# Kernel tuning notes

Measured on AMD Instinct MI355X. Metric: run time of the kernel, lower is better.

The kernel has to match this reference:

```python
import jax, jax.numpy as jnp
import numpy as np

NUM_BITS = 10
D_MODEL = 256
D_INNER = 512                      # expand=2 * hidden
D_STATE = 64
N_HEADS = 8                        # D_INNER // head_dim(64)
HEAD_DIM = 64
CONV_DIM = D_INNER + 2 * D_STATE   # 640
D_PROJ = D_INNER + CONV_DIM + N_HEADS  # 1160
KERNEL = 4
EPS = 1e-5
N_TOKENS = 16384


def _hilbert_code(coords):
    # coords: (N,3) int32 in [0, 2**NUM_BITS); Skilling's AxesToTranspose + bit interleave
    n = 3
    x = [coords[:, i] for i in range(n)]
    M = 1 << (NUM_BITS - 1)
    Q = M
    while Q > 1:
        P = Q - 1
        for i in range(n):
            cond = (x[i] & Q) > 0
            t = (x[0] ^ x[i]) & P
            x0_new = jnp.where(cond, x[0] ^ P, x[0] ^ t)
            xi_new = jnp.where(cond, x[i], x[i] ^ t)
            x[0] = x0_new
            if i > 0:
                x[i] = xi_new
        Q >>= 1
    for i in range(1, n):
        x[i] = x[i] ^ x[i - 1]
    t = jnp.zeros_like(x[0])
    Q = M
    while Q > 1:
        t = jnp.where((x[n - 1] & Q) > 0, t ^ (Q - 1), t)
        Q >>= 1
    x = [xi ^ t for xi in x]
    code = jnp.zeros_like(x[0])
    for b in range(NUM_BITS - 1, -1, -1):
        for i in range(n):
            code = (code << 1) | ((x[i] >> b) & 1)
    return code


def _serialized_orders(query_pos):
    # quantize to a 2**NUM_BITS grid, Hilbert-encode, sort ('hilbert' and 'hilbert-trans' = x/y swapped)
    pmin = query_pos.min(0)
    pmax = query_pos.max(0)
    g = ((query_pos - pmin) / (pmax - pmin + 1e-6) * (2 ** NUM_BITS - 1))
    g = jnp.clip(g, 0, 2 ** NUM_BITS - 1).astype(jnp.int32)
    orders, inverses = [], []
    for perm in ((0, 1, 2), (1, 0, 2)):
        code = _hilbert_code(g[:, jnp.array(perm)])
        o = jnp.argsort(code)
        orders.append(o)
        inverses.append(jnp.argsort(o))
    return orders, inverses


def _ln(x, w, b):
    m = x.mean(-1, keepdims=True)
    xc = x - m
    return xc * jax.lax.rsqrt(jnp.mean(xc * xc, -1, keepdims=True) + EPS) * w + b


def _mamba2(x, p):
    # x: (B, L, D_MODEL)
    B, L, _ = x.shape
    zxbcdt = x @ p['in_proj']                           # (B,L,1160)
    gate = zxbcdt[..., :D_INNER]
    xBC = zxbcdt[..., D_INNER:D_INNER + CONV_DIM]
    dt = zxbcdt[..., D_INNER + CONV_DIM:]               # (B,L,H)
    # causal depthwise conv over time
    xc = jnp.moveaxis(xBC, -1, 1)                       # (B,C,L)
    xc = jax.lax.conv_general_dilated(
        xc, p['conv_w'][:, None, :], window_strides=(1,),
        padding=[(KERNEL - 1, 0)], dimension_numbers=('NCH', 'OIH', 'NCH'),
        feature_group_count=CONV_DIM)
    xc = xc + p['conv_b'][None, :, None]
    xBC = jax.nn.silu(jnp.moveaxis(xc, 1, -1))          # (B,L,C)
    xs = xBC[..., :D_INNER].reshape(B, L, N_HEADS, HEAD_DIM)
    Bm = xBC[..., D_INNER:D_INNER + D_STATE]            # (B,L,S), n_groups=1 broadcast over heads
    Cm = xBC[..., D_INNER + D_STATE:]                   # (B,L,S)
    dt = jax.nn.softplus(dt + p['dt_bias'])             # (B,L,H)
    A = -jnp.exp(p['A_log'])                            # (H,)
    dA = jnp.exp(dt * A)                                # (B,L,H)

    def step(h, inp):
        dA_t, dt_t, x_t, B_t, C_t = inp                 # (B,H),(B,H),(B,H,P),(B,S),(B,S)
        h = h * dA_t[..., None, None] + (dt_t[..., None] * x_t)[..., None] * B_t[:, None, None, :]
        y = jnp.einsum('bhps,bs->bhp', h, C_t)
        return h, y

    tm = lambda a: jnp.moveaxis(a, 1, 0)
    h0 = jnp.zeros((B, N_HEADS, HEAD_DIM, D_STATE), x.dtype)
    _, ys = jax.lax.scan(step, h0, (tm(dA), tm(dt), tm(xs), tm(Bm), tm(Cm)))
    y = jnp.moveaxis(ys, 0, 1) + p['D'][None, None, :, None] * xs   # (B,L,H,P) + D skip
    y = y.reshape(B, L, D_INNER)
    # gated RMSNorm (MambaRMSNormGated)
    y = y * jax.nn.silu(gate)
    y = y * jax.lax.rsqrt(jnp.mean(y * y, -1, keepdims=True) + EPS) * p['norm_w']
    return y @ p['out_proj']                            # (B,L,D_MODEL)


def _forward(query, query_pos, pre_w, pre_b, fin_w, fin_b, layer_params):
    orders, invs = _serialized_orders(query_pos)
    q = query
    for p in layer_params:
        shortcut = q
        qn = _ln(q, pre_w, pre_b)
        stacked = jnp.stack([qn[orders[0]], qn[orders[1]]])   # (2, N, d) multi-path serialization
        y = _mamba2(stacked, p)
        q = shortcut + (y[0][invs[0]] + y[1][invs[1]]) * 0.5  # scatter back + average paths
        q = _ln(q, fin_w, fin_b)
    return q


def setup_inputs() -> dict:
    key = jax.random.key(0)
    ks = jax.random.split(key, 24)
    inp = {
        'query': jax.random.normal(ks[0], (N_TOKENS, D_MODEL), jnp.float32),
        'query_pos': jax.random.uniform(ks[1], (N_TOKENS, 3), jnp.float32),
        'pre_w': jnp.ones((D_MODEL,), jnp.float32),
        'pre_b': jnp.zeros((D_MODEL,), jnp.float32),
        'fin_w': jnp.ones((D_MODEL,), jnp.float32),
        'fin_b': jnp.zeros((D_MODEL,), jnp.float32),
    }
    for i in range(2):
        k = jax.random.split(ks[2 + i], 6)
        inp[f'in_proj{i}'] = jax.random.normal(k[0], (D_MODEL, D_PROJ), jnp.float32) * 0.02
        inp[f'conv_w{i}'] = jax.random.normal(k[1], (CONV_DIM, KERNEL), jnp.float32) * 0.2
        inp[f'conv_b{i}'] = jnp.zeros((CONV_DIM,), jnp.float32)
        inp[f'dt_bias{i}'] = jax.random.uniform(k[2], (N_HEADS,), jnp.float32, -4.0, -1.0)
        inp[f'A_log{i}'] = jnp.log(jnp.arange(1, N_HEADS + 1, dtype=jnp.float32))
        inp[f'D{i}'] = jnp.ones((N_HEADS,), jnp.float32)
        inp[f'norm_w{i}'] = jnp.ones((D_INNER,), jnp.float32)
        inp[f'out_proj{i}'] = jax.random.normal(k[3], (D_INNER, D_MODEL), jnp.float32) * 0.02
    return inp


def reference(query, query_pos, pre_w, pre_b, fin_w, fin_b,
              in_proj0, conv_w0, conv_b0, dt_bias0, A_log0, D0, norm_w0, out_proj0,
              in_proj1, conv_w1, conv_b1, dt_bias1, A_log1, D1, norm_w1, out_proj1):
    layer_params = [
        dict(in_proj=in_proj0, conv_w=conv_w0, conv_b=conv_b0, dt_bias=dt_bias0,
             A_log=A_log0, D=D0, norm_w=norm_w0, out_proj=out_proj0),
        dict(in_proj=in_proj1, conv_w=conv_w1, conv_b=conv_b1, dt_bias=dt_bias1,
             A_log=A_log1, D=D1, norm_w=norm_w1, out_proj=out_proj1),
    ]
    return _forward(query, query_pos, pre_w, pre_b, fin_w, fin_b, layer_params)
```

## Files before the change

kernel.cpp:

```cpp
#include <hip/hip_runtime.h>
#include <stdint.h>

#define L_TOK 16384
#define DM 256
#define DI 512
#define DS 64
#define NH 8
#define HD 64
#define CD 640
#define DP 1160
#define CHUNK 64
#define NC 256
#define EPSF 1e-5f

typedef __attribute__((ext_vector_type(8))) short short8;
typedef __attribute__((ext_vector_type(4))) float f32x4;

#define GLL16(gp, lp) __builtin_amdgcn_global_load_lds((const __attribute__((address_space(1))) void*)(gp), (__attribute__((address_space(3))) void*)(lp), 16, 0, 0)

__device__ __forceinline__ float warp_sum(float v) {
  v += __shfl_xor(v, 1, 64);
  v += __shfl_xor(v, 2, 64);
  v += __shfl_xor(v, 4, 64);
  v += __shfl_xor(v, 8, 64);
  v += __shfl_xor(v, 16, 64);
  v += __shfl_xor(v, 32, 64);
  return v;
}

__device__ __forceinline__ float siluf(float x) { return x / (1.0f + expf(-x)); }

__device__ __forceinline__ unsigned short f2bf(float f) {
  unsigned int u = __float_as_uint(f);
  unsigned int r = (u + 0x7FFFu + ((u >> 16) & 1u)) >> 16;
  return (unsigned short)r;
}
__device__ __forceinline__ float bf2f(unsigned short u) {
  return __uint_as_float(((unsigned int)u) << 16);
}


__global__ __launch_bounds__(256) void minmax_part(const float* __restrict__ pos, float* __restrict__ part) {
  __shared__ float sm[6][4];
  int tid = threadIdx.x;
  int t = blockIdx.x*256 + tid;
  float a = pos[t*3+0], b = pos[t*3+1], c = pos[t*3+2];
  float mn0=a, mn1=b, mn2=c, mx0=a, mx1=b, mx2=c;
  #pragma unroll
  for (int d = 1; d < 64; d <<= 1) {
    mn0=fminf(mn0,__shfl_xor(mn0,d,64));
    mn1=fminf(mn1,__shfl_xor(mn1,d,64));
    mn2=fminf(mn2,__shfl_xor(mn2,d,64));
    mx0=fmaxf(mx0,__shfl_xor(mx0,d,64));
    mx1=fmaxf(mx1,__shfl_xor(mx1,d,64));
    mx2=fmaxf(mx2,__shfl_xor(mx2,d,64));
  }
  if ((tid & 63) == 0) {
    int w = tid >> 6;
    sm[0][w]=mn0; sm[1][w]=mn1; sm[2][w]=mn2;
    sm[3][w]=mx0; sm[4][w]=mx1; sm[5][w]=mx2;
  }
  __syncthreads();
  if (tid < 6) {
    float r = sm[tid][0];
    if (tid < 3) { r=fminf(r,sm[tid][1]); r=fminf(r,sm[tid][2]); r=fminf(r,sm[tid][3]); }
    else         { r=fmaxf(r,sm[tid][1]); r=fmaxf(r,sm[tid][2]); r=fmaxf(r,sm[tid][3]); }
    part[blockIdx.x*6 + tid] = r;
  }
}

__global__ __launch_bounds__(64) void minmax_final(const float* __restrict__ part, float* __restrict__ pmm) {
  int tid = threadIdx.x;
  const float* p = part + tid*6;
  float mn0=p[0], mn1=p[1], mn2=p[2], mx0=p[3], mx1=p[4], mx2=p[5];
  #pragma unroll
  for (int d = 1; d < 64; d <<= 1) {
    mn0=fminf(mn0,__shfl_xor(mn0,d,64));
    mn1=fminf(mn1,__shfl_xor(mn1,d,64));
    mn2=fminf(mn2,__shfl_xor(mn2,d,64));
    mx0=fmaxf(mx0,__shfl_xor(mx0,d,64));
    mx1=fmaxf(mx1,__shfl_xor(mx1,d,64));
    mx2=fmaxf(mx2,__shfl_xor(mx2,d,64));
  }
  if (tid == 0) {
    pmm[0]=mn0; pmm[1]=mn1; pmm[2]=mn2;
    pmm[3]=mx0; pmm[4]=mx1; pmm[5]=mx2;
  }
}

__device__ unsigned int hilbert3(unsigned int a, unsigned int b, unsigned int c) {
  unsigned int x0 = a, x1 = b, x2 = c;
  for (unsigned int Q = 512u; Q > 1u; Q >>= 1) {
    unsigned int P = Q - 1u;
    { if (x0 & Q) x0 ^= P; }
    {
      unsigned int t = (x0 ^ x1) & P;
      if (x1 & Q) { x0 ^= P; }
      else { x0 ^= t; x1 ^= t; }
    }
    {
      unsigned int t = (x0 ^ x2) & P;
      if (x2 & Q) { x0 ^= P; }
      else { x0 ^= t; x2 ^= t; }
    }
  }
  x1 ^= x0; x2 ^= x1;
  unsigned int tt = 0;
  for (unsigned int Q = 512u; Q > 1u; Q >>= 1)
    if (x2 & Q) tt ^= (Q - 1u);
  x0 ^= tt; x1 ^= tt; x2 ^= tt;
  unsigned int code = 0;
  #pragma unroll
  for (int bb = 9; bb >= 0; --bb) {
    code = (code << 1) | ((x0 >> bb) & 1u);
    code = (code << 1) | ((x1 >> bb) & 1u);
    code = (code << 1) | ((x2 >> bb) & 1u);
  }
  return code;
}

__global__ __launch_bounds__(256) void hilbert_kernel(const float* __restrict__ pos, const float* __restrict__ pmm,
                                                      unsigned long long* __restrict__ keys) {
  int t = blockIdx.x*256 + threadIdx.x;
  if (t >= L_TOK) return;
  unsigned int g[3];
  #pragma unroll
  for (int d = 0; d < 3; ++d) {
    float v = (pos[t*3+d] - pmm[d]) / (pmm[3+d] - pmm[d] + 1e-6f) * 1023.0f;
    v = fminf(fmaxf(v, 0.0f), 1023.0f);
    g[d] = (unsigned int)(int)v;
  }
  unsigned int ca = hilbert3(g[0], g[1], g[2]);
  unsigned int cb = hilbert3(g[1], g[0], g[2]);
  keys[t]         = ((unsigned long long)ca << 14) | (unsigned long long)t;
  keys[L_TOK + t] = ((unsigned long long)cb << 14) | (unsigned long long)t;
}

__global__ __launch_bounds__(256) void rank_partial(const unsigned long long* __restrict__ keys,
                                                    unsigned int* __restrict__ partial) {
  __shared__ unsigned long long tile[512];
  int arr = blockIdx.y, ks = blockIdx.z;
  const unsigned long long* k = keys + (size_t)arr * L_TOK;
  int qbase = blockIdx.x*1024 + threadIdx.x;
  unsigned long long q[4];
  #pragma unroll
  for (int i = 0; i < 4; ++i) q[i] = k[qbase + 256*i];
  const unsigned long long* src = k + ks*512;
  #pragma unroll
  for (int t = 0; t < 2; ++t) tile[threadIdx.x + 256*t] = src[threadIdx.x + 256*t];
  __syncthreads();
  unsigned int r[4] = {};
  const ulonglong2* t2 = (const ulonglong2*)tile;
  #pragma unroll 4
  for (int j = 0; j < 256; ++j) {
    ulonglong2 v = t2[j];
    #pragma unroll
    for (int i = 0; i < 4; ++i) {
      r[i] += (v.x < q[i]) ? 1u : 0u;
      r[i] += (v.y < q[i]) ? 1u : 0u;
    }
  }
  #pragma unroll
  for (int i = 0; i < 4; ++i)
    partial[(size_t)(ks*2 + arr)*L_TOK + qbase + 256*i] = r[i];
}

__global__ __launch_bounds__(256) void rank_scatter(const unsigned long long* __restrict__ keys,
                                                    const unsigned int* __restrict__ partial,
                                                    unsigned int* __restrict__ ord,
                                                    unsigned int* __restrict__ inv) {
  int i = blockIdx.x*256 + threadIdx.x;
  int arr = i >> 14;
  int qi = i & (L_TOK - 1);
  unsigned int r = 0;
  #pragma unroll
  for (int ks = 0; ks < 32; ++ks) r += partial[(size_t)(ks*2 + arr)*L_TOK + qi];
  unsigned int tok = (unsigned int)(keys[i] & 0x3FFFu);
  ord[(size_t)arr*L_TOK + r] = tok;
  inv[(size_t)arr*L_TOK + tok] = r;
}


__global__ __launch_bounds__(256) void ln_kernel(const float* __restrict__ in, float* __restrict__ out,
                                                 unsigned short* __restrict__ outbf,
                                                 const float* __restrict__ w, const float* __restrict__ b) {
  int row = blockIdx.x*4 + (threadIdx.x >> 6);
  int lane = threadIdx.x & 63;
  const float4 v = *(const float4*)(in + (size_t)row*DM + lane*4);
  float s = v.x + v.y + v.z + v.w;
  float mean = warp_sum(s) * (1.0f/DM);
  float4 xc = make_float4(v.x-mean, v.y-mean, v.z-mean, v.w-mean);
  float ss = xc.x*xc.x + xc.y*xc.y + xc.z*xc.z + xc.w*xc.w;
  ss = warp_sum(ss) * (1.0f/DM);
  float inv = rsqrtf(ss + EPSF);
  const float4 w4 = *(const float4*)(w + lane*4);
  const float4 b4 = *(const float4*)(b + lane*4);
  float4 o;
  o.x = xc.x*inv*w4.x + b4.x;
  o.y = xc.y*inv*w4.y + b4.y;
  o.z = xc.z*inv*w4.z + b4.z;
  o.w = xc.w*inv*w4.w + b4.w;
  *(float4*)(out + (size_t)row*DM + lane*4) = o;
  if (outbf) {
    ushort4 ob = make_ushort4(f2bf(o.x), f2bf(o.y), f2bf(o.z), f2bf(o.w));
    *(ushort4*)(outbf + (size_t)row*DM + lane*4) = ob;
  }
}

__global__ __launch_bounds__(256) void lnfuse_kernel(float* __restrict__ io,
                                                     float* __restrict__ qn, unsigned short* __restrict__ qnbf,
                                                     const float* __restrict__ fw, const float* __restrict__ fb,
                                                     const float* __restrict__ pw, const float* __restrict__ pb) {
  int row = blockIdx.x*4 + (threadIdx.x >> 6);
  int lane = threadIdx.x & 63;
  const float4 v = *(const float4*)(io + (size_t)row*DM + lane*4);
  float s = v.x + v.y + v.z + v.w;
  float mean = warp_sum(s) * (1.0f/DM);
  float4 xc = make_float4(v.x-mean, v.y-mean, v.z-mean, v.w-mean);
  float ss = xc.x*xc.x + xc.y*xc.y + xc.z*xc.z + xc.w*xc.w;
  ss = warp_sum(ss) * (1.0f/DM);
  float inv = rsqrtf(ss + EPSF);
  const float4 w4 = *(const float4*)(fw + lane*4);
  const float4 b4 = *(const float4*)(fb + lane*4);
  float4 o;
  o.x = xc.x*inv*w4.x + b4.x;
  o.y = xc.y*inv*w4.y + b4.y;
  o.z = xc.z*inv*w4.z + b4.z;
  o.w = xc.w*inv*w4.w + b4.w;
  *(float4*)(io + (size_t)row*DM + lane*4) = o;
  if (qn) {
    float s2 = o.x + o.y + o.z + o.w;
    float mean2 = warp_sum(s2) * (1.0f/DM);
    float4 x2 = make_float4(o.x-mean2, o.y-mean2, o.z-mean2, o.w-mean2);
    float ss2 = x2.x*x2.x + x2.y*x2.y + x2.z*x2.z + x2.w*x2.w;
    ss2 = warp_sum(ss2) * (1.0f/DM);
    float inv2 = rsqrtf(ss2 + EPSF);
    const float4 pw4 = *(const float4*)(pw + lane*4);
    const float4 pb4 = *(const float4*)(pb + lane*4);
    float4 qv;
    qv.x = x2.x*inv2*pw4.x + pb4.x;
    qv.y = x2.y*inv2*pw4.y + pb4.y;
    qv.z = x2.z*inv2*pw4.z + pb4.z;
    qv.w = x2.w*inv2*pw4.w + pb4.w;
    *(float4*)(qn + (size_t)row*DM + lane*4) = qv;
    ushort4 qb = make_ushort4(f2bf(qv.x), f2bf(qv.y), f2bf(qv.z), f2bf(qv.w));
    *(ushort4*)(qnbf + (size_t)row*DM + lane*4) = qb;
  }
}


__global__ __launch_bounds__(256) void tcvt_both(const float* __restrict__ Wi, const float* __restrict__ Wo,
                                                 const float* __restrict__ nw,
                                                 unsigned short* __restrict__ WtA, unsigned short* __restrict__ WtO) {
  int idx = blockIdx.x*256 + threadIdx.x;
  if (idx < 1152*DM) {
    int n = idx >> 8, k = idx & 255;
    WtA[idx] = f2bf(Wi[(size_t)k*DP + n]);
  } else {
    int j = idx - 1152*DM;
    int n = j >> 9, k = j & 511;
    WtO[j] = f2bf(Wo[(size_t)k*DM + n] * nw[k]);
  }
}


__global__ __launch_bounds__(256) void gemm_in2(const unsigned short* __restrict__ Abf,
                                                const unsigned short* __restrict__ Wt,
                                                const unsigned int* __restrict__ ord,
                                                unsigned short* __restrict__ gate_nat,
                                                unsigned short* __restrict__ bcraw,
                                                unsigned short* __restrict__ xTg) {
  __shared__ unsigned short Alds[128*64];
  __shared__ unsigned short Blds[128*64];
  int tid = threadIdx.x, lane = tid & 63, w = tid >> 6;
  int bid = blockIdx.x;
  bool natp = bid < 640;
  int rb, cb, dir = 0, wcol0;
  if (natp) {
    int xcd = bid & 7, g = bid >> 3;
    rb = (xcd*16 + g/5)*128;
    cb = (g % 5)*128;
    wcol0 = cb;
  } else {
    int id = bid - 640;
    dir = id >> 9;
    int b = id & 511;
    int xcd = b & 7, g = b >> 3;
    rb = (xcd*16 + g/4)*128;
    cb = (g % 4)*128;
    wcol0 = DI + cb;
  }
  int wm = (w & 1)*64, wn = (w >> 1)*64;
  const unsigned int* ordp = ord + (size_t)dir*L_TOK;
  const unsigned short* pA[4]; const unsigned short* pB[4];
  unsigned short* dA[4]; unsigned short* dB[4];
  #pragma unroll
  for (int s = 0; s < 4; ++s) {
    int inst = w*4 + s;
    int r = inst*8 + (lane >> 3);
    int cA = (lane & 7) ^ (r & 7);
    int arow = natp ? (rb + r) : (int)ordp[rb + r];
    pA[s] = Abf + (size_t)arow*DM + cA*8;
    pB[s] = Wt + (size_t)(wcol0 + r)*DM + cA*8;
    dA[s] = &Alds[inst*512];
    dB[s] = &Blds[inst*512];
  }
  f32x4 zero = {0.f, 0.f, 0.f, 0.f};
  f32x4 acc[4][4];
  #pragma unroll
  for (int i = 0; i < 4; ++i)
    #pragma unroll
    for (int j = 0; j < 4; ++j) acc[i][j] = zero;
  int t = lane & 15, q = lane >> 4;
  for (int k0 = 0; k0 < DM; k0 += 64) {
    #pragma unroll
    for (int s = 0; s < 4; ++s) GLL16(pA[s] + k0, dA[s]);
    #pragma unroll
    for (int s = 0; s < 4; ++s) GLL16(pB[s] + k0, dB[s]);
    __syncthreads();
    #pragma unroll
    for (int ks = 0; ks < 2; ++ks) {
      short8 af[4], bfr[4];
      int cc = ks*4 + q;
      #pragma unroll
      for (int i = 0; i < 4; ++i) {
        int rr = wm + 16*i + t;
        af[i] = *(const short8*)&Alds[rr*64 + ((cc ^ (rr & 7))*8)];
      }
      #pragma unroll
      for (int j = 0; j < 4; ++j) {
        int rr = wn + 16*j + t;
        bfr[j] = *(const short8*)&Blds[rr*64 + ((cc ^ (rr & 7))*8)];
      }
      #pragma unroll
      for (int i = 0; i < 4; ++i)
        #pragma unroll
        for (int j = 0; j < 4; ++j)
          acc[i][j] = __builtin_amdgcn_mfma_f32_16x16x32_bf16(af[i], bfr[j], acc[i][j], 0, 0, 0);
    }
    __syncthreads();
  }
  if (natp) {
    unsigned short* dst; int ld;
    if (cb < DI) { dst = gate_nat + cb; ld = DI; }
    else         { dst = bcraw + (cb - DI); ld = 128; }
    #pragma unroll
    for (int i = 0; i < 4; ++i) {
      int rowb = rb + wm + 16*i + q*4;
      #pragma unroll
      for (int j = 0; j < 4; ++j) {
        int col = wn + 16*j + t;
        #pragma unroll
        for (int r = 0; r < 4; ++r)
          dst[(size_t)(rowb + r)*ld + col] = f2bf(acc[i][j][r]);
      }
    }
  } else {
    #pragma unroll
    for (int i = 0; i < 4; ++i) {
      int rowb = rb + wm + 16*i + q*4;
      #pragma unroll
      for (int j = 0; j < 4; ++j) {
        int col = wn + 16*j + t;
        ushort4 o = make_ushort4(f2bf(acc[i][j][0]), f2bf(acc[i][j][1]),
                                 f2bf(acc[i][j][2]), f2bf(acc[i][j][3]));
        *(ushort4*)(xTg + (size_t)(cb + col)*(2*L_TOK) + (size_t)dir*L_TOK + rowb) = o;
      }
    }
  }
}


__global__ __launch_bounds__(256) void gemm_out_gather(const unsigned short* __restrict__ ybuf,
                                                       const unsigned short* __restrict__ Wt,
                                                       const unsigned int* __restrict__ inv,
                                                       const float* __restrict__ rms_acc,
                                                       const float* __restrict__ shortcut,
                                                       float* __restrict__ out) {
  __shared__ unsigned short Alds[2*64*64];
  __shared__ unsigned short Blds[128*64];
  int tid = threadIdx.x, lane = tid & 63, w = tid >> 6;
  int bid = blockIdx.x;
  int xcd = bid & 7, g = bid >> 3;
  int rb = (xcd*32 + (g >> 1))*64;
  int cb = (g & 1)*128;
  int wm = (w & 1)*32, wn = (w >> 1)*64;
  const unsigned short* pA0[2]; const unsigned short* pA1[2];
  unsigned short* dA0[2]; unsigned short* dA1[2];
  const unsigned short* pB[4]; unsigned short* dB[4];
  #pragma unroll
  for (int s = 0; s < 2; ++s) {
    int inst = w*2 + s;
    int r = inst*8 + (lane >> 3);
    int cA = (lane & 7) ^ (r & 7);
    int tok = rb + r;
    pA0[s] = ybuf + (size_t)inv[tok]*DI + cA*8;
    pA1[s] = ybuf + (size_t)L_TOK*DI + (size_t)inv[L_TOK + tok]*DI + cA*8;
    dA0[s] = &Alds[inst*512];
    dA1[s] = &Alds[4096 + inst*512];
  }
  #pragma unroll
  for (int s = 0; s < 4; ++s) {
    int inst = w*4 + s;
    int r = inst*8 + (lane >> 3);
    int cA = (lane & 7) ^ (r & 7);
    pB[s] = Wt + (size_t)(cb + r)*DI + cA*8;
    dB[s] = &Blds[inst*512];
  }
  f32x4 zero = {0.f, 0.f, 0.f, 0.f};
  f32x4 acc0[2][4], acc1[2][4];
  #pragma unroll
  for (int i = 0; i < 2; ++i)
    #pragma unroll
    for (int j = 0; j < 4; ++j) { acc0[i][j] = zero; acc1[i][j] = zero; }
  int t = lane & 15, q = lane >> 4;
  for (int k0 = 0; k0 < DI; k0 += 64) {
    #pragma unroll
    for (int s = 0; s < 2; ++s) { GLL16(pA0[s] + k0, dA0[s]); GLL16(pA1[s] + k0, dA1[s]); }
    #pragma unroll
    for (int s = 0; s < 4; ++s) GLL16(pB[s] + k0, dB[s]);
    __syncthreads();
    #pragma unroll
    for (int ks = 0; ks < 2; ++ks) {
      short8 af0[2], af1[2], bfr[4];
      int cc = ks*4 + q;
      #pragma unroll
      for (int i = 0; i < 2; ++i) {
        int rr = wm + 16*i + t;
        int off = rr*64 + ((cc ^ (rr & 7))*8);
        af0[i] = *(const short8*)&Alds[off];
        af1[i] = *(const short8*)&Alds[4096 + off];
      }
      #pragma unroll
      for (int j = 0; j < 4; ++j) {
        int rr = wn + 16*j + t;
        bfr[j] = *(const short8*)&Blds[rr*64 + ((cc ^ (rr & 7))*8)];
      }
      #pragma unroll
      for (int i = 0; i < 2; ++i)
        #pragma unroll
        for (int j = 0; j < 4; ++j) {
          acc0[i][j] = __builtin_amdgcn_mfma_f32_16x16x32_bf16(af0[i], bfr[j], acc0[i][j], 0, 0, 0);
          acc1[i][j] = __builtin_amdgcn_mfma_f32_16x16x32_bf16(af1[i], bfr[j], acc1[i][j], 0, 0, 0);
        }
    }
    __syncthreads();
  }
  #pragma unroll
  for (int i = 0; i < 2; ++i) {
    #pragma unroll
    for (int r = 0; r < 4; ++r) {
      int row = rb + wm + 16*i + q*4 + r;
      float ir0 = rsqrtf(rms_acc[row]*(1.0f/DI) + EPSF);
      float ir1 = rsqrtf(rms_acc[L_TOK + row]*(1.0f/DI) + EPSF);
      const float* sp = shortcut + (size_t)row*DM + cb;
      float* op = out + (size_t)row*DM + cb;
      #pragma unroll
      for (int j = 0; j < 4; ++j) {
        int col = wn + 16*j + t;
        op[col] = sp[col] + 0.5f*(ir0*acc0[i][j][r] + ir1*acc1[i][j][r]);
      }
    }
  }
}


__global__ __launch_bounds__(256) void dtconv(const float* __restrict__ qn, const float* __restrict__ W,
                                              const float* __restrict__ dt_bias, float* __restrict__ dtb,
                                              float* __restrict__ rms_acc,
                                              const unsigned short* __restrict__ bcraw,
                                              const float* __restrict__ cw, const float* __restrict__ cbias,
                                              const unsigned int* __restrict__ ord,
                                              unsigned short* __restrict__ bcswz,
                                              unsigned short* __restrict__ bcswzA) {
  __shared__ unsigned short smem[131*64];
  int tid = threadIdx.x;
  int bx = blockIdx.x;
  if (bx < 512) {
    int gid = bx*256 + tid;
    if (gid < 2*L_TOK) rms_acc[gid] = 0.f;
    float* Wl = (float*)smem;
    {
      const float* wp = W + (size_t)tid*DP + (DI + CD);
      float4 wa = *(const float4*)wp;
      float4 wb = *(const float4*)(wp + 4);
      int off = tid*8 + (tid >> 5)*4;
      *(float4*)&Wl[off]     = wa;
      *(float4*)&Wl[off + 4] = wb;
    }
    __syncthreads();
    int lane = tid & 63, w = tid >> 6;
    int r = bx*32 + w*8 + (lane >> 3);
    int kg = lane & 7;
    const float* qp = qn + (size_t)r*DM + kg*32;
    float acc[8] = {};
    #pragma unroll
    for (int i = 0; i < 8; ++i) {
      float4 q4 = *(const float4*)(qp + i*4);
      float qv[4] = {q4.x, q4.y, q4.z, q4.w};
      #pragma unroll
      for (int e = 0; e < 4; ++e) {
        int k = kg*32 + i*4 + e;
        int off = k*8 + kg*4;
        float4 wa = *(const float4*)&Wl[off];
        float4 wb = *(const float4*)&Wl[off + 4];
        acc[0] = fmaf(qv[e], wa.x, acc[0]);
        acc[1] = fmaf(qv[e], wa.y, acc[1]);
        acc[2] = fmaf(qv[e], wa.z, acc[2]);
        acc[3] = fmaf(qv[e], wa.w, acc[3]);
        acc[4] = fmaf(qv[e], wb.x, acc[4]);
        acc[5] = fmaf(qv[e], wb.y, acc[5]);
        acc[6] = fmaf(qv[e], wb.z, acc[6]);
        acc[7] = fmaf(qv[e], wb.w, acc[7]);
      }
    }
    #pragma unroll
    for (int h = 0; h < 8; ++h) {
      acc[h] += __shfl_xor(acc[h], 8, 64);
      acc[h] += __shfl_xor(acc[h], 16, 64);
      acc[h] += __shfl_xor(acc[h], 32, 64);
    }
    float v = 0.f;
    #pragma unroll
    for (int h = 0; h < 8; ++h) if (kg == h) v = acc[h];
    v += dt_bias[kg];
    float sp = (v > 0.0f) ? (v + log1pf(expf(-v))) : log1pf(expf(v));
    dtb[(size_t)r*NH + kg] = sp;
  } else {
    int cid = bx - 512;
    int half = cid & 1, ty = (cid >> 1) & 127, dir = cid >> 8;
    unsigned short* tile = smem;
    const unsigned int* ordp = ord + (size_t)dir*L_TOK;
    int ch0 = DI + half*64;
    int co0 = half*64;
    int t0 = ty*128;
    for (int cc = tid; cc < 131*8; cc += 256) {
      int r = cc >> 3, cgc = cc & 7;
      int t = t0 - 3 + r;
      short8 v = {0,0,0,0,0,0,0,0};
      if (t >= 0) v = *(const short8*)(bcraw + (size_t)ordp[t]*128 + co0 + cgc*8);
      *(short8*)&tile[r*64 + ((cgc ^ (r & 7))*8)] = v;
    }
    int cg = tid & 7, tp = tid >> 3;
    int ch = ch0 + cg*8;
    float wv[8][4];
    float bias[8];
    #pragma unroll
    for (int e = 0; e < 8; ++e) {
      float4 c4 = *(const float4*)(cw + (ch + e)*4);
      wv[e][0] = c4.x; wv[e][1] = c4.y; wv[e][2] = c4.z; wv[e][3] = c4.w;
    }
    {
      float4 b0 = *(const float4*)(cbias + ch);
      float4 b1 = *(const float4*)(cbias + ch + 4);
      bias[0]=b0.x; bias[1]=b0.y; bias[2]=b0.z; bias[3]=b0.w;
      bias[4]=b1.x; bias[5]=b1.y; bias[6]=b1.z; bias[7]=b1.w;
    }
    __syncthreads();
    #pragma unroll
    for (int tk = 0; tk < 4; ++tk) {
      int rel = tp + 32*tk;
      float acc[8];
      #pragma unroll
      for (int e = 0; e < 8; ++e) acc[e] = bias[e];
      #pragma unroll
      for (int k = 0; k < 4; ++k) {
        int r = rel + k;
        short8 v = *(const short8*)&tile[r*64 + ((cg ^ (r & 7))*8)];
        #pragma unroll
        for (int e = 0; e < 8; ++e)
          acc[e] = fmaf(wv[e][k], bf2f((unsigned short)v[e]), acc[e]);
      }
      short8 o;
      #pragma unroll
      for (int e = 0; e < 8; ++e) o[e] = (short)f2bf(siluf(acc[e]));
      int T = t0 + rel;
      int chn = T >> 6, tl = T & 63;
      unsigned short* tb = bcswz + ((size_t)((dir*NC + chn)*2 + half))*4096;
      *(short8*)(tb + tl*64 + ((cg ^ (tl & 7))*8)) = o;
      if (half == 0) {
        unsigned short* ta = bcswzA + ((size_t)(dir*NC + chn))*4096;
        #pragma unroll
        for (int e = 0; e < 8; ++e) {
          int s5 = cg*8 + e;
          ta[s5*64 + (((tl >> 3) ^ (s5 & 7))*8) + (tl & 7)] = (unsigned short)o[e];
        }
      }
    }
  }
}


__global__ __launch_bounds__(256) void phaseA_mfma(const unsigned short* __restrict__ xTg,
                                                   const unsigned short* __restrict__ bcswzA,
                                                   const float* __restrict__ cw, const float* __restrict__ cbias,
                                                   const float* __restrict__ dtb, const float* __restrict__ A_log,
                                                   const unsigned int* __restrict__ ord,
                                                   unsigned short* __restrict__ S, float* __restrict__ P,
                                                   unsigned short* __restrict__ xsT) {
  int c = blockIdx.x, h = blockIdx.y, dir = blockIdx.z, tid = threadIdx.x;
  int lane = tid & 63, w = tid >> 6;
  int hh = dir*NH + h;
  __shared__ unsigned short xT[64*64];
  __shared__ unsigned short Bt[64*64];
  __shared__ float wgt[64];
  int c0 = c*CHUNK;
  float Ah = -expf(A_log[h]);
  const unsigned short* bA = bcswzA + ((size_t)(dir*NC + c))*4096;
  #pragma unroll
  for (int s = 0; s < 2; ++s) {
    int inst = w*2 + s;
    GLL16(bA + (size_t)inst*512 + lane*8, &Bt[inst*512]);
  }
  if (tid < 64) {
    unsigned int tok = ord[(size_t)dir*L_TOK + c0 + tid];
    float dtv = dtb[(size_t)tok*NH + h];
    float v = dtv*Ah;
    float s = v;
    #pragma unroll
    for (int d = 1; d < 64; d <<= 1) {
      float u = __shfl_down(s, d, 64);
      s += (tid + d < 64) ? u : 0.f;
    }
    wgt[tid] = dtv*expf(s - v);
    if (tid == 0) P[hh*NC + c] = expf(s);
  }
  __syncthreads();
  unsigned short* xpg = xsT + ((size_t)(hh*NC + c))*4096;
  #pragma unroll
  for (int i = 0; i < 2; ++i) {
    int q = tid + 256*i;
    int p = q >> 3, tg = q & 7;
    int sw8 = (tg ^ (p & 7))*8;
    const unsigned short* xrow = xTg + (size_t)(h*HD + p)*(2*L_TOK) + (size_t)dir*L_TOK;
    int tb = c0 + tg*8;
    short8 cur = *(const short8*)(xrow + tb);
    short8 prv = {0,0,0,0,0,0,0,0};
    if (tb >= 8) prv = *(const short8*)(xrow + tb - 8);
    float4 w4 = *(const float4*)(cw + (size_t)(h*HD + p)*4);
    float bb = cbias[h*HD + p];
    float xv[11];
    xv[0] = bf2f((unsigned short)prv[5]);
    xv[1] = bf2f((unsigned short)prv[6]);
    xv[2] = bf2f((unsigned short)prv[7]);
    #pragma unroll
    for (int k = 0; k < 8; ++k) xv[3+k] = bf2f((unsigned short)cur[k]);
    short8 raw, wtd;
    #pragma unroll
    for (int k = 0; k < 8; ++k) {
      float a = bb + w4.x*xv[k] + w4.y*xv[k+1] + w4.z*xv[k+2] + w4.w*xv[k+3];
      unsigned short rbf = f2bf(siluf(a));
      raw[k] = (short)rbf;
      wtd[k] = (short)f2bf(bf2f(rbf)*wgt[tg*8 + k]);
    }
    *(short8*)(xpg + p*64 + sw8) = raw;
    *(short8*)&xT[p*64 + sw8] = wtd;
  }
  __syncthreads();
  int t16 = lane & 15, q4 = lane >> 4;
  f32x4 zero = {0.f,0.f,0.f,0.f};
  f32x4 acc[4];
  #pragma unroll
  for (int j = 0; j < 4; ++j) acc[j] = zero;
  #pragma unroll
  for (int ks = 0; ks < 2; ++ks) {
    int rowA = 16*w + t16;
    short8 a = *(const short8*)&xT[rowA*64 + (((ks*4 + q4) ^ (rowA & 7))*8)];
    #pragma unroll
    for (int j = 0; j < 4; ++j) {
      int rowB = 16*j + t16;
      short8 b = *(const short8*)&Bt[rowB*64 + (((ks*4 + q4) ^ (rowB & 7))*8)];
      acc[j] = __builtin_amdgcn_mfma_f32_16x16x32_bf16(a, b, acc[j], 0, 0, 0);
    }
  }
  unsigned short* Sp = S + ((size_t)(hh*NC + c))*4096;
  #pragma unroll
  for (int j = 0; j < 4; ++j)
    #pragma unroll
    for (int r = 0; r < 4; ++r) {
      int row = 16*w + q4*4 + r;
      int cg2 = 2*j + (t16 >> 3);
      Sp[(size_t)row*64 + (((cg2 ^ (row & 7)) << 3) | (t16 & 7))] = f2bf(acc[j][r]);
    }
}


__global__ __launch_bounds__(128) void phaseB_scan(unsigned short* __restrict__ S, const float* __restrict__ P) {
  __shared__ float Pl[NC];
  int b = blockIdx.x;
  int hh = b >> 4;
  int e2 = (b & 15)*128 + threadIdx.x;
  for (int i = threadIdx.x; i < NC; i += 128) Pl[i] = P[hh*NC + i];
  __syncthreads();
  unsigned int* base = (unsigned int*)(S + ((size_t)hh*NC)*4096) + e2;
  float hx = 0.f, hy = 0.f;
  #pragma unroll 1
  for (int k0 = 0; k0 < NC; k0 += 16) {
    unsigned int v[16];
    #pragma unroll
    for (int u = 0; u < 16; ++u) v[u] = base[(size_t)(k0+u)*2048];
    #pragma unroll
    for (int u = 0; u < 16; ++u) {
      float p = Pl[k0+u];
      unsigned int old = v[u];
      base[(size_t)(k0+u)*2048] = (unsigned int)f2bf(hx) | ((unsigned int)f2bf(hy) << 16);
      hx = p*hx + bf2f((unsigned short)(old & 0xffffu));
      hy = p*hy + bf2f((unsigned short)(old >> 16));
    }
  }
}

__global__ __launch_bounds__(256) void phaseC_mfma(const unsigned short* __restrict__ bcswz,
                                                   const unsigned short* __restrict__ xsT,
                                                   const unsigned short* __restrict__ gate_nat,
                                                   const float* __restrict__ dtb, const float* __restrict__ A_log,
                                                   const float* __restrict__ Dp,
                                                   const unsigned int* __restrict__ ord,
                                                   const unsigned short* __restrict__ S,
                                                   unsigned short* __restrict__ ybuf,
                                                   float* __restrict__ rms_acc) {
  int c = blockIdx.x, h = blockIdx.y, dir = blockIdx.z, tid = threadIdx.x;
  int lane = tid & 63, w = tid >> 6;
  int hh = dir*NH + h;
  unsigned short* y = ybuf + (size_t)dir*L_TOK*DI;
  __shared__ unsigned short Cl[64*64];
  __shared__ unsigned short Bl[64*64];
  __shared__ unsigned short h0l[64*64];
  __shared__ unsigned short xT[64*64];
  __shared__ float dts[64], pl[64], pe[64];
  int c0 = c*CHUNK;
  float Ah = -expf(A_log[h]);
  float Dh = Dp[h];
  const unsigned short* Sp = S + ((size_t)(hh*NC + c))*4096;
  const unsigned short* xp = xsT + ((size_t)(hh*NC + c))*4096;
  const unsigned short* Bg = bcswz + ((size_t)((dir*NC + c)*2 + 0))*4096;
  const unsigned short* Cg = bcswz + ((size_t)((dir*NC + c)*2 + 1))*4096;
  #pragma unroll
  for (int s = 0; s < 2; ++s) {
    int inst = w*2 + s;
    GLL16(Sp + (size_t)inst*512 + lane*8, &h0l[inst*512]);
    GLL16(xp + (size_t)inst*512 + lane*8, &xT[inst*512]);
    GLL16(Bg + (size_t)inst*512 + lane*8, &Bl[inst*512]);
    GLL16(Cg + (size_t)inst*512 + lane*8, &Cl[inst*512]);
  }
  if (tid < 64) {
    unsigned int tok = ord[(size_t)dir*L_TOK + c0 + tid];
    float dtv = dtb[(size_t)tok*NH + h];
    dts[tid] = dtv;
    float v = dtv*Ah;
    float s = v;
    #pragma unroll
    for (int d = 1; d < 64; d <<= 1) {
      float u = __shfl_up(s, d, 64);
      s += (tid >= d) ? u : 0.f;
    }
    pl[tid] = s;
    pe[tid] = expf(s);
  }
  __syncthreads();
  int t16 = lane & 15, q4 = lane >> 4;
  int t0 = 16*w;
  f32x4 zero = {0.f,0.f,0.f,0.f};
  f32x4 accG[4], accY[4];
  #pragma unroll
  for (int j = 0; j < 4; ++j) { accG[j] = zero; accY[j] = zero; }
  #pragma unroll
  for (int ks = 0; ks < 2; ++ks) {
    int rowA = t0 + t16;
    short8 a = *(const short8*)&Cl[rowA*64 + (((ks*4 + q4) ^ (rowA & 7))*8)];
    #pragma unroll
    for (int j = 0; j < 4; ++j) {
      int rowB = 16*j + t16;
      int off = rowB*64 + (((ks*4 + q4) ^ (rowB & 7))*8);
      accG[j] = __builtin_amdgcn_mfma_f32_16x16x32_bf16(a, *(const short8*)&Bl[off], accG[j], 0, 0, 0);
      accY[j] = __builtin_amdgcn_mfma_f32_16x16x32_bf16(a, *(const short8*)&h0l[off], accY[j], 0, 0, 0);
    }
  }
  #pragma unroll
  for (int j = 0; j < 4; ++j) {
    #pragma unroll
    for (int r = 0; r < 4; ++r) {
      int t = t0 + q4*4 + r;
      int s = 16*j + t16;
      float v = 0.f;
      if (s <= t) {
        v = accG[j][r] * dts[s] * expf(pl[t] - pl[s]);
        if (s == t) v += Dh;
      }
      Cl[t*64 + (((s >> 3) ^ (t & 7))*8 + (s & 7))] = f2bf(v);
    }
  }
  unsigned int tokr[4];
  #pragma unroll
  for (int r = 0; r < 4; ++r) tokr[r] = ord[(size_t)dir*L_TOK + c0 + t0 + q4*4 + r];
  float gv[4][4];
  #pragma unroll
  for (int r = 0; r < 4; ++r)
    #pragma unroll
    for (int j = 0; j < 4; ++j)
      gv[r][j] = bf2f(gate_nat[(size_t)tokr[r]*DI + h*HD + 16*j + t16]);
  #pragma unroll
  for (int j = 0; j < 4; ++j)
    #pragma unroll
    for (int r = 0; r < 4; ++r)
      accY[j][r] *= pe[t0 + q4*4 + r];
  #pragma unroll
  for (int ks = 0; ks < 2; ++ks) {
    int rowA = t0 + t16;
    short8 a = *(const short8*)&Cl[rowA*64 + (((ks*4 + q4) ^ (rowA & 7))*8)];
    #pragma unroll
    for (int j = 0; j < 4; ++j) {
      int rowB = 16*j + t16;
      short8 b = *(const short8*)&xT[rowB*64 + (((ks*4 + q4) ^ (rowB & 7))*8)];
      accY[j] = __builtin_amdgcn_mfma_f32_16x16x32_bf16(a, b, accY[j], 0, 0, 0);
    }
  }
  float sq[4] = {0.f, 0.f, 0.f, 0.f};
  #pragma unroll
  for (int j = 0; j < 4; ++j)
    #pragma unroll
    for (int r = 0; r < 4; ++r) {
      float val = accY[j][r] * siluf(gv[r][j]);
      int t = t0 + q4*4 + r;
      int p = 16*j + t16;
      y[(size_t)(c0+t)*DI + h*HD + p] = f2bf(val);
      sq[r] += val*val;
    }
  #pragma unroll
  for (int r = 0; r < 4; ++r) {
    float s2 = sq[r];
    s2 += __shfl_xor(s2, 1, 64);
    s2 += __shfl_xor(s2, 2, 64);
    s2 += __shfl_xor(s2, 4, 64);
    s2 += __shfl_xor(s2, 8, 64);
    if (t16 == 0) atomicAdd(&rms_acc[(size_t)dir*L_TOK + tokr[r]], s2);
  }
}

__global__ void fill_debug(float* out, float v) {
  int i = blockIdx.x*256 + threadIdx.x;
  if (i < L_TOK*DM) out[i] = v;
}


extern "C" void kernel_launch(void* const* d_in, const int* in_sizes, int n_in,
                              void* d_out, int out_size, void* d_ws, size_t ws_size,
                              hipStream_t stream) {
  const float* query = (const float*)d_in[0];
  const float* qpos  = (const float*)d_in[1];
  const float* pre_w = (const float*)d_in[2];
  const float* pre_b = (const float*)d_in[3];
  const float* fin_w = (const float*)d_in[4];
  const float* fin_b = (const float*)d_in[5];
  float* out = (float*)d_out;

  char* ws = (char*)d_ws;
  size_t off = 0;
  auto alloc = [&](size_t bytes) -> void* {
    void* p = ws + off;
    off += (bytes + 255) & ~(size_t)255;
    return p;
  };
  unsigned long long* keys = (unsigned long long*)alloc((size_t)2*L_TOK*8);
  unsigned int* ord = (unsigned int*)alloc((size_t)2*L_TOK*4);
  unsigned int* inv = (unsigned int*)alloc((size_t)2*L_TOK*4);
  unsigned int* rpart = (unsigned int*)alloc((size_t)32*2*L_TOK*4);
  float* pmm  = (float*)alloc(256);
  float* mmpart = (float*)alloc((size_t)64*6*4);
  float* qn   = (float*)alloc((size_t)L_TOK*DM*4);
  unsigned short* qnbf = (unsigned short*)alloc((size_t)L_TOK*DM*2);
  unsigned short* gate_nat = (unsigned short*)alloc((size_t)L_TOK*DI*2);
  unsigned short* xTg    = (unsigned short*)alloc((size_t)512*2*L_TOK*2);
  unsigned short* bcraw  = (unsigned short*)alloc((size_t)L_TOK*128*2);
  unsigned short* bcswz  = (unsigned short*)alloc((size_t)2*NC*2*4096*2);
  unsigned short* bcswzA = (unsigned short*)alloc((size_t)2*NC*4096*2);
  unsigned short* ybuf   = (unsigned short*)alloc((size_t)2*L_TOK*DI*2);
  float* dtb  = (float*)alloc((size_t)L_TOK*NH*4);
  float* rms_acc = (float*)alloc((size_t)2*L_TOK*4);
  unsigned short* Sbuf = (unsigned short*)alloc((size_t)2*NH*NC*4096*2);
  unsigned short* xsT  = (unsigned short*)alloc((size_t)2*NH*NC*4096*2);
  float* Pbuf = (float*)alloc((size_t)2*NH*NC*4);
  unsigned short* WtA = (unsigned short*)alloc((size_t)1152*DM*2);
  unsigned short* WtO = (unsigned short*)alloc((size_t)DM*DI*2);
  if (off > ws_size) {
    fill_debug<<<(L_TOK*DM + 255)/256, 256, 0, stream>>>(out, (float)(ws_size >> 20));
    return;
  }

  minmax_part<<<64, 256, 0, stream>>>(qpos, mmpart);
  minmax_final<<<1, 64, 0, stream>>>(mmpart, pmm);
  hilbert_kernel<<<L_TOK/256, 256, 0, stream>>>(qpos, pmm, keys);
  rank_partial<<<dim3(16, 2, 32), 256, 0, stream>>>(keys, rpart);
  rank_scatter<<<(2*L_TOK)/256, 256, 0, stream>>>(keys, rpart, ord, inv);

  for (int l = 0; l < 2; ++l) {
    int base = 6 + 8*l;
    const float* in_proj  = (const float*)d_in[base+0];
    const float* conv_w   = (const float*)d_in[base+1];
    const float* conv_b   = (const float*)d_in[base+2];
    const float* dt_bias  = (const float*)d_in[base+3];
    const float* A_log    = (const float*)d_in[base+4];
    const float* Dp       = (const float*)d_in[base+5];
    const float* norm_w   = (const float*)d_in[base+6];
    const float* out_proj = (const float*)d_in[base+7];

    if (l == 0)
      ln_kernel<<<L_TOK/4, 256, 0, stream>>>(query, qn, qnbf, pre_w, pre_b);
    tcvt_both<<<(1152*DM + DM*DI)/256, 256, 0, stream>>>(in_proj, out_proj, norm_w, WtA, WtO);
    gemm_in2<<<1664, 256, 0, stream>>>(qnbf, WtA, ord, gate_nat, bcraw, xTg);
    dtconv<<<1024, 256, 0, stream>>>(qn, in_proj, dt_bias, dtb, rms_acc,
                                     bcraw, conv_w, conv_b, ord, bcswz, bcswzA);
    phaseA_mfma<<<dim3(NC, NH, 2), 256, 0, stream>>>(xTg, bcswzA, conv_w, conv_b, dtb, A_log, ord, Sbuf, Pbuf, xsT);
    phaseB_scan<<<256, 128, 0, stream>>>(Sbuf, Pbuf);
    phaseC_mfma<<<dim3(NC, NH, 2), 256, 0, stream>>>(bcswz, xsT, gate_nat, dtb, A_log, Dp, ord, Sbuf, ybuf, rms_acc);
    gemm_out_gather<<<512, 256, 0, stream>>>(ybuf, WtO, inv, rms_acc,
                                             l ? (const float*)out : query, out);
    if (l == 0)
      lnfuse_kernel<<<L_TOK/4, 256, 0, stream>>>(out, qn, qnbf, fin_w, fin_b, pre_w, pre_b);
    else
      lnfuse_kernel<<<L_TOK/4, 256, 0, stream>>>(out, nullptr, nullptr, fin_w, fin_b, pre_w, pre_b);
  }
}
```

Before: 490.8 us.

## Vectorize phaseC epilogue via LDS transpose and use fast exp/silu intrinsics

The phaseC epilogue now stages the fp32 accumulators through swizzled shared memory (reusing the h0l/xT space) so each thread writes 16 contiguous bf16 outputs as two 16-byte stores. The gate values are fetched early with vector loads to overlap with the MFMA work, and the per-token RMS atomics drop from one per 16-lane group to one per 4-thread group. Separately, expf and the silu division are replaced with __expf and a hardware reciprocal in several kernels. This adds two barriers and slightly lowers exp/silu precision.

```diff
diff --git a/kernel.cpp b/kernel.cpp
--- a/kernel.cpp
+++ b/kernel.cpp
@@ -28,6 +28,8 @@
   return v;
 }
 
+__device__ __forceinline__ float fexp(float x) { return __expf(x); }
+__device__ __forceinline__ float fsilu(float x) { return x * __builtin_amdgcn_rcpf(1.0f + __expf(-x)); }
 __device__ __forceinline__ float siluf(float x) { return x / (1.0f + expf(-x)); }
 
 __device__ __forceinline__ unsigned short f2bf(float f) {
@@ -524,7 +526,7 @@
     #pragma unroll
     for (int h = 0; h < 8; ++h) if (kg == h) v = acc[h];
     v += dt_bias[kg];
-    float sp = (v > 0.0f) ? (v + log1pf(expf(-v))) : log1pf(expf(v));
+    float sp = (v > 0.0f) ? (v + log1pf(__expf(-v))) : log1pf(__expf(v));
     dtb[(size_t)r*NH + kg] = sp;
   } else {
     int cid = bx - 512;
@@ -573,7 +575,7 @@
       }
       short8 o;
       #pragma unroll
-      for (int e = 0; e < 8; ++e) o[e] = (short)f2bf(siluf(acc[e]));
+      for (int e = 0; e < 8; ++e) o[e] = (short)f2bf(fsilu(acc[e]));
       int T = t0 + rel;
       int chn = T >> 6, tl = T & 63;
       unsigned short* tb = bcswz + ((size_t)((dir*NC + chn)*2 + half))*4096;
@@ -622,8 +624,8 @@
       float u = __shfl_down(s, d, 64);
       s += (tid + d < 64) ? u : 0.f;
     }
-    wgt[tid] = dtv*expf(s - v);
-    if (tid == 0) P[hh*NC + c] = expf(s);
+    wgt[tid] = dtv*fexp(s - v);
+    if (tid == 0) P[hh*NC + c] = fexp(s);
   }
   __syncthreads();
   unsigned short* xpg = xsT + ((size_t)(hh*NC + c))*4096;
@@ -649,7 +651,7 @@
     #pragma unroll
     for (int k = 0; k < 8; ++k) {
       float a = bb + w4.x*xv[k] + w4.y*xv[k+1] + w4.z*xv[k+2] + w4.w*xv[k+3];
-      unsigned short rbf = f2bf(siluf(a));
+      unsigned short rbf = f2bf(fsilu(a));
       raw[k] = (short)rbf;
       wtd[k] = (short)f2bf(bf2f(rbf)*wgt[tg*8 + k]);
     }
@@ -723,11 +725,13 @@
   int lane = tid & 63, w = tid >> 6;
   int hh = dir*NH + h;
   unsigned short* y = ybuf + (size_t)dir*L_TOK*DI;
-  __shared__ unsigned short Cl[64*64];
-  __shared__ unsigned short Bl[64*64];
-  __shared__ unsigned short h0l[64*64];
-  __shared__ unsigned short xT[64*64];
+  __shared__ __align__(16) unsigned short smemT[4*4096];
   __shared__ float dts[64], pl[64], pe[64];
+  unsigned short* Cl  = smemT;
+  unsigned short* Bl  = smemT + 4096;
+  unsigned short* h0l = smemT + 8192;
+  unsigned short* xT  = smemT + 12288;
+  float* fT = (float*)(smemT + 8192);
   int c0 = c*CHUNK;
   float Ah = -expf(A_log[h]);
   float Dh = Dp[h];
@@ -743,6 +747,12 @@
     GLL16(Bg + (size_t)inst*512 + lane*8, &Bl[inst*512]);
     GLL16(Cg + (size_t)inst*512 + lane*8, &Cl[inst*512]);
   }
+  int erow = tid >> 2;
+  int ech0 = (tid & 3) * 16;
+  unsigned int etok = ord[(size_t)dir*L_TOK + c0 + erow];
+  const unsigned short* gp = gate_nat + (size_t)etok*DI + h*HD + ech0;
+  short8 g0 = *(const short8*)gp;
+  short8 g1 = *(const short8*)(gp + 8);
   if (tid < 64) {
     unsigned int tok = ord[(size_t)dir*L_TOK + c0 + tid];
     float dtv = dtb[(size_t)tok*NH + h];
@@ -755,7 +765,7 @@
       s += (tid >= d) ? u : 0.f;
     }
     pl[tid] = s;
-    pe[tid] = expf(s);
+    pe[tid] = fexp(s);
   }
   __syncthreads();
   int t16 = lane & 15, q4 = lane >> 4;
@@ -784,21 +794,12 @@
       int s = 16*j + t16;
       float v = 0.f;
       if (s <= t) {
-        v = accG[j][r] * dts[s] * expf(pl[t] - pl[s]);
+        v = accG[j][r] * dts[s] * fexp(pl[t] - pl[s]);
         if (s == t) v += Dh;
       }
       Cl[t*64 + (((s >> 3) ^ (t & 7))*8 + (s & 7))] = f2bf(v);
     }
   }
-  unsigned int tokr[4];
-  #pragma unroll
-  for (int r = 0; r < 4; ++r) tokr[r] = ord[(size_t)dir*L_TOK + c0 + t0 + q4*4 + r];
-  float gv[4][4];
-  #pragma unroll
-  for (int r = 0; r < 4; ++r)
-    #pragma unroll
-    for (int j = 0; j < 4; ++j)
-      gv[r][j] = bf2f(gate_nat[(size_t)tokr[r]*DI + h*HD + 16*j + t16]);
   #pragma unroll
   for (int j = 0; j < 4; ++j)
     #pragma unroll
@@ -815,25 +816,41 @@
       accY[j] = __builtin_amdgcn_mfma_f32_16x16x32_bf16(a, b, accY[j], 0, 0, 0);
     }
   }
-  float sq[4] = {0.f, 0.f, 0.f, 0.f};
+  __syncthreads();
   #pragma unroll
   for (int j = 0; j < 4; ++j)
     #pragma unroll
     for (int r = 0; r < 4; ++r) {
-      float val = accY[j][r] * siluf(gv[r][j]);
       int t = t0 + q4*4 + r;
       int p = 16*j + t16;
-      y[(size_t)(c0+t)*DI + h*HD + p] = f2bf(val);
-      sq[r] += val*val;
-    }
-  #pragma unroll
-  for (int r = 0; r < 4; ++r) {
-    float s2 = sq[r];
-    s2 += __shfl_xor(s2, 1, 64);
-    s2 += __shfl_xor(s2, 2, 64);
-    s2 += __shfl_xor(s2, 4, 64);
-    s2 += __shfl_xor(s2, 8, 64);
-    if (t16 == 0) atomicAdd(&rms_acc[(size_t)dir*L_TOK + tokr[r]], s2);
+      fT[t*64 + (p ^ (q4 << 4))] = accY[j][r];
+    }
+  __syncthreads();
+  {
+    int swz = ((erow >> 2) & 3) << 4;
+    const float* fr = &fT[erow*64 + (ech0 ^ swz)];
+    float4 a0 = *(const float4*)(fr);
+    float4 a1 = *(const float4*)(fr + 4);
+    float4 a2 = *(const float4*)(fr + 8);
+    float4 a3 = *(const float4*)(fr + 12);
+    float fv[16] = {a0.x,a0.y,a0.z,a0.w, a1.x,a1.y,a1.z,a1.w,
+                    a2.x,a2.y,a2.z,a2.w, a3.x,a3.y,a3.z,a3.w};
+    float sq = 0.f;
+    short8 o0, o1;
+    #pragma unroll
+    for (int e = 0; e < 8; ++e) {
+      float v0 = fv[e]   * fsilu(bf2f((unsigned short)g0[e]));
+      float v1 = fv[8+e] * fsilu(bf2f((unsigned short)g1[e]));
+      o0[e] = (short)f2bf(v0);
+      o1[e] = (short)f2bf(v1);
+      sq += v0*v0 + v1*v1;
+    }
+    unsigned short* yp = y + (size_t)(c0 + erow)*DI + h*HD + ech0;
+    *(short8*)yp = o0;
+    *(short8*)(yp + 8) = o1;
+    sq += __shfl_xor(sq, 1, 64);
+    sq += __shfl_xor(sq, 2, 64);
+    if ((tid & 3) == 0) atomicAdd(&rms_acc[(size_t)dir*L_TOK + etok], sq);
   }
 }
 
```

Result: faster. 470.8 us (-4.1%).
